# Kernel optimization log

Measured on AMD Instinct MI355X. Metric: run time of the kernel, lower is better.

The kernel has to match this reference:

```python
import jax, jax.numpy as jnp
import numpy as np

B, S, H = 1024, 512, 768
NUM_CLASSES = 3


def setup_inputs() -> dict:
    key = jax.random.key(0)
    k1, k2, k3, k4 = jax.random.split(key, 4)
    embeddings = jax.random.normal(k1, (B, S, H), dtype=jnp.float32)
    # labels 0..4; 2/3/4 mark pronoun, entity A, entity B tokens
    mentions = jax.random.randint(k2, (B, S), 0, 5, dtype=jnp.int64)
    W1 = jax.random.normal(k3, (3 * H, 512), dtype=jnp.float32) * 0.02
    b1 = jnp.zeros((512,), dtype=jnp.float32)
    W2 = jax.random.normal(k4, (512, NUM_CLASSES), dtype=jnp.float32) * 0.02
    b2 = jnp.zeros((NUM_CLASSES,), dtype=jnp.float32)
    return {"embeddings": embeddings, "mentions": mentions,
            "W1": W1, "b1": b1, "W2": W2, "b2": b2}


def _masked_mean(embeddings, mentions, label):
    # embeddings: [B,S,H], mentions: [B,S] -> [B,H]
    mask = (mentions == label).astype(embeddings.dtype)  # [B,S]
    s = jnp.einsum('bsh,bs->bh', embeddings, mask)
    c = jnp.sum(mask, axis=1, keepdims=True)             # [B,1]
    return s / c


def reference(embeddings, mentions, W1, b1, W2, b2):
    # Dropout is identity in eval mode. Vectorized replacement of the
    # python loop + growing torch.cat: three segment-mean pools, concat,
    # then 2-layer MLP classifier.
    pronouns = _masked_mean(embeddings, mentions, 2)
    entities_a = _masked_mean(embeddings, mentions, 3)
    entities_b = _masked_mean(embeddings, mentions, 4)
    o = jnp.concatenate([pronouns, entities_a, entities_b], axis=-1)  # [B,3H]
    h = jax.nn.relu(o @ W1 + b1)
    return h @ W2 + b2
```

## Files before the change

### kernel.cpp

```cpp
#include <hip/hip_runtime.h>
#include <hip/hip_bf16.h>

#define B_SZ 1024
#define S_SZ 512
#define H_SZ 768
#define K3H  2304
#define HID  512
#define NC   3
#define KSPLIT_HALF 1152

typedef __attribute__((ext_vector_type(8)))  __bf16        bf16x8;
typedef __attribute__((ext_vector_type(16))) float         f32x16;
typedef __attribute__((ext_vector_type(8)))  unsigned short ushort8x;

__device__ __forceinline__ unsigned short f2bf(float f) {
    unsigned u = __builtin_bit_cast(unsigned, f);
    unsigned r = (u + 0x7fffu + ((u >> 16) & 1u)) >> 16;
    return (unsigned short)r;
}

__global__ __launch_bounds__(192) void pool_tr_kernel(
        const float* __restrict__ emb,
        const int*   __restrict__ men,
        const float* __restrict__ W1,
        unsigned short* __restrict__ o,
        unsigned short* __restrict__ Bt)
{
    const int t = threadIdx.x;

    if (blockIdx.x >= B_SZ) {
        __shared__ unsigned short tile[64][65];
        const int bt = blockIdx.x - B_SZ;
        const int kb = (bt >> 3) * 64;
        const int nb = (bt & 7) * 64;
        for (int i = t; i < 4096; i += 192) {
            int r = i >> 6, c = i & 63;
            tile[r][c] = f2bf(W1[(size_t)(kb + r) * HID + nb + c]);
        }
        __syncthreads();
        for (int i = t; i < 4096; i += 192) {
            int rr = i >> 6, cc = i & 63;
            Bt[(size_t)(nb + rr) * K3H + kb + cc] = tile[cc][rr];
        }
        return;
    }

    const int b = blockIdx.x;
    __shared__ unsigned short sel[S_SZ];
    __shared__ int nsel_sh;
    __shared__ int cnt[3];

    if (t < 64) {
        int basep = 0;
        int c0 = 0, c1 = 0, c2 = 0;
        #pragma unroll
        for (int ch = 0; ch < 8; ++ch) {
            int s = ch * 64 + t;
            int m = men[(size_t)b * S_SZ + s];
            bool pick = (m >= 2);
            unsigned long long mk = __ballot(pick);
            int pos = basep + __popcll(mk & ((1ull << t) - 1ull));
            if (pick) sel[pos] = (unsigned short)(s | ((m - 2) << 12));
            basep += __popcll(mk);
            c0 += (m == 2);
            c1 += (m == 3);
            c2 += (m == 4);
        }
        #pragma unroll
        for (int off = 32; off > 0; off >>= 1) {
            c0 += __shfl_down(c0, off);
            c1 += __shfl_down(c1, off);
            c2 += __shfl_down(c2, off);
        }
        if (t == 0) { nsel_sh = basep; cnt[0] = c0; cnt[1] = c1; cnt[2] = c2; }
    }
    __syncthreads();

    const int ns = nsel_sh;
    float4 a0 = {0.f,0.f,0.f,0.f}, a1 = {0.f,0.f,0.f,0.f}, a2 = {0.f,0.f,0.f,0.f};
    const float4* base =
        reinterpret_cast<const float4*>(emb + (size_t)b * S_SZ * H_SZ);

    #define ACCUM(E, V) do {                                             \
        int tg_ = (E) >> 12;                                             \
        if (tg_ == 0)      { a0.x+=V.x; a0.y+=V.y; a0.z+=V.z; a0.w+=V.w; } \
        else if (tg_ == 1) { a1.x+=V.x; a1.y+=V.y; a1.z+=V.z; a1.w+=V.w; } \
        else               { a2.x+=V.x; a2.y+=V.y; a2.z+=V.z; a2.w+=V.w; } \
    } while (0)

    int i = 0;
    for (; i + 4 <= ns; i += 4) {
        int e0 = sel[i], e1 = sel[i+1], e2 = sel[i+2], e3 = sel[i+3];
        float4 v0 = base[(e0 & 0x1ff) * 192 + t];
        float4 v1 = base[(e1 & 0x1ff) * 192 + t];
        float4 v2 = base[(e2 & 0x1ff) * 192 + t];
        float4 v3 = base[(e3 & 0x1ff) * 192 + t];
        ACCUM(e0, v0); ACCUM(e1, v1); ACCUM(e2, v2); ACCUM(e3, v3);
    }
    for (; i < ns; ++i) {
        int e = sel[i];
        float4 v = base[(e & 0x1ff) * 192 + t];
        ACCUM(e, v);
    }
    #undef ACCUM

    const float r0 = 1.f / (float)cnt[0];
    const float r1 = 1.f / (float)cnt[1];
    const float r2 = 1.f / (float)cnt[2];

    unsigned short* op = o + (size_t)b * K3H;
    ushort4 w0 = { f2bf(a0.x*r0), f2bf(a0.y*r0), f2bf(a0.z*r0), f2bf(a0.w*r0) };
    ushort4 w1 = { f2bf(a1.x*r1), f2bf(a1.y*r1), f2bf(a1.z*r1), f2bf(a1.w*r1) };
    ushort4 w2 = { f2bf(a2.x*r2), f2bf(a2.y*r2), f2bf(a2.z*r2), f2bf(a2.w*r2) };
    *reinterpret_cast<ushort4*>(op + 0 * H_SZ + t * 4) = w0;
    *reinterpret_cast<ushort4*>(op + 1 * H_SZ + t * 4) = w1;
    *reinterpret_cast<ushort4*>(op + 2 * H_SZ + t * 4) = w2;
}

__global__ __launch_bounds__(256) void mlp1_kernel(
        const unsigned short* __restrict__ A,
        const unsigned short* __restrict__ Bt,
        float*       __restrict__ hp)
{
    __shared__ unsigned short lds[2][2][64 * 64];

    const int t  = threadIdx.x;
    const int m0 = blockIdx.y * 64;
    const int n0 = blockIdx.x * 64;
    const int kz = blockIdx.z;
    const int kbase = kz * KSPLIT_HALF;

    const int w  = t >> 6, l = t & 63;
    const int wr = w >> 1, wc = w & 1;
    const int lr = l & 31;
    const int hi = l >> 5;
    const int sw = lr & 7;

    const int s_row0 = t >> 3;
    const int s_row1 = 32 + (t >> 3);
    const int s_slot = t & 7;

    const unsigned short* a_p0 = A  + (size_t)(m0 + s_row0) * K3H + kbase + s_slot * 8;
    const unsigned short* a_p1 = A  + (size_t)(m0 + s_row1) * K3H + kbase + s_slot * 8;
    const unsigned short* b_p0 = Bt + (size_t)(n0 + s_row0) * K3H + kbase + s_slot * 8;
    const unsigned short* b_p1 = Bt + (size_t)(n0 + s_row1) * K3H + kbase + s_slot * 8;

    const int w_idx0 = s_row0 * 64 + ((s_slot ^ (s_row0 & 7)) * 8);
    const int w_idx1 = s_row1 * 64 + ((s_slot ^ (s_row1 & 7)) * 8);

    f32x16 acc = {0.f,0.f,0.f,0.f,0.f,0.f,0.f,0.f,
                  0.f,0.f,0.f,0.f,0.f,0.f,0.f,0.f};

    ushort8x ra0 = *(const ushort8x*)(a_p0);
    ushort8x ra1 = *(const ushort8x*)(a_p1);
    ushort8x rb0 = *(const ushort8x*)(b_p0);
    ushort8x rb1 = *(const ushort8x*)(b_p1);
    *(ushort8x*)&lds[0][0][w_idx0] = ra0;
    *(ushort8x*)&lds[0][0][w_idx1] = ra1;
    *(ushort8x*)&lds[0][1][w_idx0] = rb0;
    *(ushort8x*)&lds[0][1][w_idx1] = rb1;
    __syncthreads();

    const int NT = KSPLIT_HALF / 64;
    int cur = 0;
    const int a_frag_row = (wr * 32 + lr) * 64;
    const int b_frag_row = (wc * 32 + lr) * 64;

    for (int step = 0; step < NT; ++step) {
        if (step + 1 < NT) {
            const size_t koff = (size_t)(step + 1) * 64;
            ra0 = *(const ushort8x*)(a_p0 + koff);
            ra1 = *(const ushort8x*)(a_p1 + koff);
            rb0 = *(const ushort8x*)(b_p0 + koff);
            rb1 = *(const ushort8x*)(b_p1 + koff);
        }

        const unsigned short* As = lds[cur][0];
        const unsigned short* Bs = lds[cur][1];
        #pragma unroll
        for (int kk = 0; kk < 64; kk += 16) {
            const int ks = (kk >> 3) + hi;
            bf16x8 af = *(const bf16x8*)&As[a_frag_row + ((ks ^ sw) * 8)];
            bf16x8 bf = *(const bf16x8*)&Bs[b_frag_row + ((ks ^ sw) * 8)];
            acc = __builtin_amdgcn_mfma_f32_32x32x16_bf16(af, bf, acc, 0, 0, 0);
        }
        __syncthreads();

        if (step + 1 < NT) {
            const int nb = cur ^ 1;
            *(ushort8x*)&lds[nb][0][w_idx0] = ra0;
            *(ushort8x*)&lds[nb][0][w_idx1] = ra1;
            *(ushort8x*)&lds[nb][1][w_idx0] = rb0;
            *(ushort8x*)&lds[nb][1][w_idx1] = rb1;
            __syncthreads();
            cur = nb;
        }
    }

    float* out = hp + (size_t)kz * B_SZ * HID;
    const int col = n0 + wc * 32 + lr;
    #pragma unroll
    for (int r = 0; r < 16; ++r) {
        int row = (r & 3) + 8 * (r >> 2) + 4 * hi;
        out[(size_t)(m0 + wr * 32 + row) * HID + col] = acc[r];
    }
}

__global__ __launch_bounds__(256) void mlp2_kernel(
        const float* __restrict__ hp,
        const float* __restrict__ b1,
        const float* __restrict__ W2,
        const float* __restrict__ b2,
        float*       __restrict__ out)
{
    const int w = threadIdx.x >> 6;
    const int l = threadIdx.x & 63;
    const int b = blockIdx.x * 4 + w;

    const float* h0 = hp + (size_t)b * HID;
    const float* h1 = hp + (size_t)B_SZ * HID + (size_t)b * HID;

    float a0 = 0.f, a1 = 0.f, a2 = 0.f;
    #pragma unroll
    for (int kk = 0; kk < HID; kk += 64) {
        int k = kk + l;
        float hv = fmaxf(h0[k] + h1[k] + b1[k], 0.f);
        a0 += hv * W2[k * 3 + 0];
        a1 += hv * W2[k * 3 + 1];
        a2 += hv * W2[k * 3 + 2];
    }
    #pragma unroll
    for (int off = 32; off > 0; off >>= 1) {
        a0 += __shfl_down(a0, off);
        a1 += __shfl_down(a1, off);
        a2 += __shfl_down(a2, off);
    }
    if (l == 0) {
        out[b * 3 + 0] = a0 + b2[0];
        out[b * 3 + 1] = a1 + b2[1];
        out[b * 3 + 2] = a2 + b2[2];
    }
}

extern "C" void kernel_launch(void* const* d_in, const int* in_sizes, int n_in,
                              void* d_out, int out_size, void* d_ws, size_t ws_size,
                              hipStream_t stream) {
    const float* emb = (const float*)d_in[0];
    const int*   men = (const int*)  d_in[1];
    const float* W1  = (const float*)d_in[2];
    const float* b1  = (const float*)d_in[3];
    const float* W2  = (const float*)d_in[4];
    const float* b2  = (const float*)d_in[5];
    float* out = (float*)d_out;

    unsigned short* o_bf = (unsigned short*)d_ws;
    unsigned short* w1t  = o_bf + (size_t)B_SZ * K3H;
    float*          hp   = (float*)(w1t + (size_t)HID * K3H);

    pool_tr_kernel<<<B_SZ + 288, 192, 0, stream>>>(emb, men, W1, o_bf, w1t);
    mlp1_kernel<<<dim3(8, 16, 2), 256, 0, stream>>>(o_bf, w1t, hp);
    mlp2_kernel<<<256, 256, 0, stream>>>(hp, b1, W2, b2, out);
}
```

Before: 197.8 us.

## Split pooling per batch into three single-wave blocks over H chunks

The pooling work for each batch row is split across three 64-thread blocks, each covering a 256-wide slice of H, instead of one 192-thread block. Each wave now scans the mentions itself with per-label ballots, so the shared count array and the shared selected-count broadcast go away. The W1 transpose blocks are rewritten for 64 threads. The change raises block count and latency hiding for the gather, but the mention scan is repeated three times per batch row.

```diff
diff --git a/kernel.cpp b/kernel.cpp
--- a/kernel.cpp
+++ b/kernel.cpp
@@ -8,6 +8,7 @@
 #define HID  512
 #define NC   3
 #define KSPLIT_HALF 1152
+#define POOL_BLKS (B_SZ * 3)
 
 typedef __attribute__((ext_vector_type(8)))  __bf16        bf16x8;
 typedef __attribute__((ext_vector_type(16))) float         f32x16;
@@ -19,67 +20,61 @@
     return (unsigned short)r;
 }
 
-__global__ __launch_bounds__(192) void pool_tr_kernel(
+__global__ __launch_bounds__(64) void pool_tr_kernel(
         const float* __restrict__ emb,
         const int*   __restrict__ men,
         const float* __restrict__ W1,
         unsigned short* __restrict__ o,
         unsigned short* __restrict__ Bt)
 {
-    const int t = threadIdx.x;
-
-    if (blockIdx.x >= B_SZ) {
+    const int t   = threadIdx.x;
+    const int blk = blockIdx.x;
+
+    if (blk >= POOL_BLKS) {
         __shared__ unsigned short tile[64][65];
-        const int bt = blockIdx.x - B_SZ;
+        const int bt = blk - POOL_BLKS;
         const int kb = (bt >> 3) * 64;
         const int nb = (bt & 7) * 64;
-        for (int i = t; i < 4096; i += 192) {
-            int r = i >> 6, c = i & 63;
-            tile[r][c] = f2bf(W1[(size_t)(kb + r) * HID + nb + c]);
-        }
+        #pragma unroll 4
+        for (int r = 0; r < 64; ++r)
+            tile[r][t] = f2bf(W1[(size_t)(kb + r) * HID + nb + t]);
         __syncthreads();
-        for (int i = t; i < 4096; i += 192) {
-            int rr = i >> 6, cc = i & 63;
-            Bt[(size_t)(nb + rr) * K3H + kb + cc] = tile[cc][rr];
-        }
+        #pragma unroll 4
+        for (int r = 0; r < 64; ++r)
+            Bt[(size_t)(nb + r) * K3H + kb + t] = tile[t][r];
         return;
     }
 
-    const int b = blockIdx.x;
+    const int b  = blk / 3;
+    const int cz = blk - b * 3;
+
     __shared__ unsigned short sel[S_SZ];
-    __shared__ int nsel_sh;
-    __shared__ int cnt[3];
-
-    if (t < 64) {
-        int basep = 0;
-        int c0 = 0, c1 = 0, c2 = 0;
-        #pragma unroll
-        for (int ch = 0; ch < 8; ++ch) {
-            int s = ch * 64 + t;
-            int m = men[(size_t)b * S_SZ + s];
-            bool pick = (m >= 2);
-            unsigned long long mk = __ballot(pick);
-            int pos = basep + __popcll(mk & ((1ull << t) - 1ull));
-            if (pick) sel[pos] = (unsigned short)(s | ((m - 2) << 12));
-            basep += __popcll(mk);
-            c0 += (m == 2);
-            c1 += (m == 3);
-            c2 += (m == 4);
-        }
-        #pragma unroll
-        for (int off = 32; off > 0; off >>= 1) {
-            c0 += __shfl_down(c0, off);
-            c1 += __shfl_down(c1, off);
-            c2 += __shfl_down(c2, off);
-        }
-        if (t == 0) { nsel_sh = basep; cnt[0] = c0; cnt[1] = c1; cnt[2] = c2; }
+
+    int basep = 0;
+    int c0 = 0, c1 = 0, c2 = 0;
+    const unsigned long long lt = (1ull << t) - 1ull;
+    #pragma unroll
+    for (int ch = 0; ch < 8; ++ch) {
+        int s = ch * 64 + t;
+        int m = men[(size_t)b * S_SZ + s];
+        unsigned long long k2 = __ballot(m == 2);
+        unsigned long long k3 = __ballot(m == 3);
+        unsigned long long k4 = __ballot(m == 4);
+        unsigned long long pk = k2 | k3 | k4;
+        int pos = basep + __popcll(pk & lt);
+        if (m >= 2) sel[pos] = (unsigned short)(s | ((m - 2) << 12));
+        basep += __popcll(pk);
+        c0 += __popcll(k2);
+        c1 += __popcll(k3);
+        c2 += __popcll(k4);
     }
     __syncthreads();
 
-    const int ns = nsel_sh;
+    const int ns = basep;
     float4 a0 = {0.f,0.f,0.f,0.f}, a1 = {0.f,0.f,0.f,0.f}, a2 = {0.f,0.f,0.f,0.f};
     const float4* base =
-        reinterpret_cast<const float4*>(emb + (size_t)b * S_SZ * H_SZ);
+        reinterpret_cast<const float4*>(emb + (size_t)b * S_SZ * H_SZ)
+        + cz * 64 + t;
 
     #define ACCUM(E, V) do {                                             \
         int tg_ = (E) >> 12;                                             \
@@ -91,30 +86,30 @@
     int i = 0;
     for (; i + 4 <= ns; i += 4) {
         int e0 = sel[i], e1 = sel[i+1], e2 = sel[i+2], e3 = sel[i+3];
-        float4 v0 = base[(e0 & 0x1ff) * 192 + t];
-        float4 v1 = base[(e1 & 0x1ff) * 192 + t];
-        float4 v2 = base[(e2 & 0x1ff) * 192 + t];
-        float4 v3 = base[(e3 & 0x1ff) * 192 + t];
+        float4 v0 = base[(e0 & 0x1ff) * 192];
+        float4 v1 = base[(e1 & 0x1ff) * 192];
+        float4 v2 = base[(e2 & 0x1ff) * 192];
+        float4 v3 = base[(e3 & 0x1ff) * 192];
         ACCUM(e0, v0); ACCUM(e1, v1); ACCUM(e2, v2); ACCUM(e3, v3);
     }
     for (; i < ns; ++i) {
         int e = sel[i];
-        float4 v = base[(e & 0x1ff) * 192 + t];
+        float4 v = base[(e & 0x1ff) * 192];
         ACCUM(e, v);
     }
     #undef ACCUM
 
-    const float r0 = 1.f / (float)cnt[0];
-    const float r1 = 1.f / (float)cnt[1];
-    const float r2 = 1.f / (float)cnt[2];
-
-    unsigned short* op = o + (size_t)b * K3H;
+    const float r0 = 1.f / (float)c0;
+    const float r1 = 1.f / (float)c1;
+    const float r2 = 1.f / (float)c2;
+
+    unsigned short* op = o + (size_t)b * K3H + cz * 256 + t * 4;
     ushort4 w0 = { f2bf(a0.x*r0), f2bf(a0.y*r0), f2bf(a0.z*r0), f2bf(a0.w*r0) };
     ushort4 w1 = { f2bf(a1.x*r1), f2bf(a1.y*r1), f2bf(a1.z*r1), f2bf(a1.w*r1) };
     ushort4 w2 = { f2bf(a2.x*r2), f2bf(a2.y*r2), f2bf(a2.z*r2), f2bf(a2.w*r2) };
-    *reinterpret_cast<ushort4*>(op + 0 * H_SZ + t * 4) = w0;
-    *reinterpret_cast<ushort4*>(op + 1 * H_SZ + t * 4) = w1;
-    *reinterpret_cast<ushort4*>(op + 2 * H_SZ + t * 4) = w2;
+    *reinterpret_cast<ushort4*>(op + 0 * H_SZ) = w0;
+    *reinterpret_cast<ushort4*>(op + 1 * H_SZ) = w1;
+    *reinterpret_cast<ushort4*>(op + 2 * H_SZ) = w2;
 }
 
 __global__ __launch_bounds__(256) void mlp1_kernel(
@@ -257,7 +252,7 @@
     unsigned short* w1t  = o_bf + (size_t)B_SZ * K3H;
     float*          hp   = (float*)(w1t + (size_t)HID * K3H);
 
-    pool_tr_kernel<<<B_SZ + 288, 192, 0, stream>>>(emb, men, W1, o_bf, w1t);
+    pool_tr_kernel<<<POOL_BLKS + 288, 64, 0, stream>>>(emb, men, W1, o_bf, w1t);
     mlp1_kernel<<<dim3(8, 16, 2), 256, 0, stream>>>(o_bf, w1t, hp);
     mlp2_kernel<<<256, 256, 0, stream>>>(hp, b1, W2, b2, out);
 }
```

New measurement: 199.1 us. Within noise of the previous version (+0.7%).
